# Performance work log

Measured on AMD Instinct MI355X. Metric: run time of the kernel, lower is better.

Reference implementation:

```python
import jax, jax.numpy as jnp
import numpy as np

WS = 8          # window_size
POOL = 7        # int(sqrt(agent_num=49)) -> AdaptiveAvgPool1d output size


def _pool_matrix(L, p):
    """Averaging matrix [L, p] replicating torch AdaptiveAvgPool1d(L -> p)."""
    starts = np.floor(np.arange(p) * L / p).astype(int)
    ends = np.ceil((np.arange(p) + 1) * L / p).astype(int)
    P = np.zeros((L, p), dtype=np.float32)
    for i in range(p):
        P[starts[i]:ends[i], i] = 1.0 / (ends[i] - starts[i])
    return jnp.asarray(P)


def setup_inputs() -> dict:
    key = jax.random.key(0)
    ks = jax.random.split(key, 4)
    B, C, H, W = 8, 96, 192, 192
    s = 1.0 / np.sqrt(C)
    return {
        "x": jax.random.normal(ks[0], (B, C, H, W), jnp.float32),
        "Wv": jax.random.normal(ks[1], (C, C), jnp.float32) * s,
        "bv": jnp.zeros((C,), jnp.float32),
        "Wq": jax.random.normal(ks[2], (C, C), jnp.float32) * s,
        "bq": jnp.zeros((C,), jnp.float32),
        "Wk": jax.random.normal(ks[3], (C, C), jnp.float32) * s,
        "bk": jnp.zeros((C,), jnp.float32),
    }


def _conv1x1(x, Wt, b):
    # Conv2d(dim, dim, 1): weight [out, in]
    return jnp.einsum('bchw,oc->bohw', x, Wt) + b[None, :, None, None]


def reference(x, Wv, bv, Wq, bq, Wk, bk):
    B, C, H, W = x.shape
    ws = WS
    nh, nw = H // ws, W // ws
    L = ws * ws  # tokens per window (64)

    v = _conv1x1(x, Wv, bv)
    q = _conv1x1(x, Wq, bq)
    k = _conv1x1(x, Wk, bk)

    def win(t):  # b c (h dh) (w dw) -> (b h w) (dh dw) c
        t = t.reshape(B, C, nh, ws, nw, ws)
        return t.transpose(0, 2, 4, 3, 5, 1).reshape(B * nh * nw, L, C)

    vw, qw, kw = win(v), win(q), win(k)  # (N, 64, C) each

    # agent tokens: adaptive avg pool over the 64 in-window positions -> 7
    P = _pool_matrix(L, POOL)
    agent = jnp.einsum('nlc,lp->npc', qw, P)  # (N, 7, C)

    # agent attention (attn_drop = 0 -> identity)
    a_attn = jax.nn.softmax(jnp.einsum('npc,nlc->npl', agent, kw), axis=-1)
    agent_v = jnp.einsum('npl,nlc->npc', a_attn, vw)            # (N, 7, C)
    q_attn = jax.nn.softmax(jnp.einsum('nlc,npc->nlp', qw, agent), axis=-1)
    f = jnp.einsum('nlp,npc->nlc', q_attn, agent_v)             # (N, 64, C)

    # (b h w) (dh dw) c -> b c (h dh) (w dw)
    out = f.reshape(B, nh, nw, ws, ws, C).transpose(0, 5, 1, 3, 2, 4)
    return out.reshape(B, C, H, W)
```

## Files before the change

### kernel.cpp

```cpp
#include <hip/hip_runtime.h>


constexpr int C_   = 96;
constexpr int Wimg = 192;
constexpr int HWp  = 192 * 192;
constexpr int NWIN = 24;
constexpr int Pp   = 7;

typedef __attribute__((ext_vector_type(8))) __bf16 bf16x8;
typedef __attribute__((ext_vector_type(4))) __bf16 bf16x4;
typedef __attribute__((ext_vector_type(8))) short  short8;
typedef __attribute__((ext_vector_type(4))) float  f32x4;
union frag_u { short8 s; bf16x8 b; };

constexpr int XWS   = 0;
constexpr int XWLC  = 12288;
constexpr int R1    = 24768;
constexpr int R2    = 31168;
constexpr int QATB  = 37568;
constexpr int SMEMB = 39872;

constexpr int WS_FRAG_BYTE = 18944 * 4;
constexpr int WS_WV_BYTE   = WS_FRAG_BYTE + 84 * 1024;


__device__ __forceinline__ void hilo8(const float4 a, const float4 b,
                                      frag_u& H, frag_u& L) {
    float v[8] = {a.x, a.y, a.z, a.w, b.x, b.y, b.z, b.w};
    #pragma unroll
    for (int j = 0; j < 8; ++j) {
        const __bf16 h = (__bf16)v[j];
        H.b[j] = h;
        L.b[j] = (__bf16)(v[j] - (float)h);
    }
}

__device__ __forceinline__ short8 xws_fragA(const unsigned char* S, int mt, int ks, int lane) {
    const int c  = mt * 16 + (lane & 15);
    const int l2 = ks * 64 + ((lane >> 4) << 4);
    return *reinterpret_cast<const short8*>(S + XWS + c * 128 + (l2 ^ ((c & 7) << 4)));
}


__global__ void precompute_mats(const float* __restrict__ Wq,
                                const float* __restrict__ Wk,
                                float* __restrict__ Mk,
                                float* __restrict__ Mq)
{
    const int c  = blockIdx.x;
    const int cp = threadIdx.x;
    float ak = 0.f, aq = 0.f;
    for (int a = 0; a < C_; ++a) {
        const float wq = Wq[a * C_ + c];
        ak = fmaf(wq, Wk[a * C_ + cp], ak);
        aq = fmaf(wq, Wq[a * C_ + cp], aq);
    }
    Mk[c * C_ + cp] = ak;
    Mq[c * C_ + cp] = aq;
}

__global__ void precompute_vecs(const float* __restrict__ Wq,
                                const float* __restrict__ Wk,
                                const float* __restrict__ bq,
                                const float* __restrict__ bk,
                                float* __restrict__ uk,  float* __restrict__ uq,
                                float* __restrict__ bk2, float* __restrict__ bq2,
                                float* __restrict__ scal)
{
    const int c = threadIdx.x;
    float a_uk = 0.f, a_uq = 0.f, a_bk2 = 0.f, a_bq2 = 0.f;
    for (int a = 0; a < C_; ++a) {
        const float wqc = Wq[a * C_ + c];
        a_uk  = fmaf(wqc, bk[a], a_uk);
        a_uq  = fmaf(wqc, bq[a], a_uq);
        a_bk2 = fmaf(bq[a], Wk[a * C_ + c], a_bk2);
        a_bq2 = fmaf(bq[a], Wq[a * C_ + c], a_bq2);
    }
    uk[c] = a_uk; uq[c] = a_uq; bk2[c] = a_bk2; bq2[c] = a_bq2;
    if (c == 0) {
        float sk = 0.f, sq = 0.f;
        for (int a = 0; a < C_; ++a) { sk += bq[a] * bk[a]; sq += bq[a] * bq[a]; }
        scal[0] = sk; scal[1] = sq;
    }
}

__global__ void precompute_frags(const float* __restrict__ ws,
                                 const float* __restrict__ Wv,
                                 unsigned char* __restrict__ wsb)
{
    const int bid = blockIdx.x, lane = threadIdx.x;
    short8 o;
    if (bid < 84) {
        const int hl = bid & 1, ks = (bid >> 1) % 3, nt = (bid / 6) % 7, mat = bid / 42;
        const float* M = ws + (mat ? 9216 : 0);
        const float* u = ws + (mat ? 18528 : 18432);
        const int col = nt * 16 + (lane & 15);
        #pragma unroll
        for (int j = 0; j < 8; ++j) {
            const int k = ks * 32 + (lane >> 4) * 8 + j;
            const float raw = (col < 96) ? M[k * 96 + col] : ((col == 96) ? u[k] : 0.f);
            const __bf16 hi = (__bf16)raw;
            union { __bf16 h; short s; } cv;
            cv.h = hl ? (__bf16)(raw - (float)hi) : hi;
            o[j] = cv.s;
        }
        *reinterpret_cast<short8*>(wsb + WS_FRAG_BYTE + bid * 1024 + lane * 16) = o;
    } else {
        const int wb = bid - 84;
        const int hl = wb & 1, ks = (wb >> 1) % 3, mt = wb / 6;
        const int row = mt * 16 + (lane & 15);
        #pragma unroll
        for (int j = 0; j < 8; ++j) {
            const int c = ks * 32 + (lane >> 4) * 8 + j;
            const float raw = Wv[row * 96 + c];
            const __bf16 hi = (__bf16)raw;
            union { __bf16 h; short s; } cv;
            cv.h = hl ? (__bf16)(raw - (float)hi) : hi;
            o[j] = cv.s;
        }
        *reinterpret_cast<short8*>(wsb + WS_WV_BYTE + wb * 1024 + lane * 16) = o;
    }
}


__global__ __launch_bounds__(256, 4) void camixer_main(
    const float* __restrict__ x,
    const float* __restrict__ bv,
    const float* __restrict__ bk2,
    const float* __restrict__ bq2,
    const float* __restrict__ scal,
    const unsigned char* __restrict__ mfrag,
    const unsigned char* __restrict__ wvfrag,
    float* __restrict__ out)
{
    __shared__ __align__(16) unsigned char S[SMEMB];
    float* xpf  = (float*)(S + R1);
    float* Lraw = (float*)(S + R1);
    float* xvf  = (float*)(S + R1);
    float* gkq  = (float*)(S + R2);
    float* avT  = (float*)(S + R2);
    float* qat  = (float*)(S + QATB);

    const int t = threadIdx.x;
    const int lane = t & 63, w = t >> 6;
    const int wid = ((blockIdx.x & 7) * 576) + (blockIdx.x >> 3);
    const int b  = wid / (NWIN * NWIN);
    const int r  = wid % (NWIN * NWIN);
    const int h0 = (r / NWIN) * 8;
    const int w0 = (r % NWIN) * 8;
    const int base = b * C_ * HWp + h0 * Wimg + w0;
    const float scal0 = scal[0], scal1 = scal[1];

    {
        const float4* x4 = reinterpret_cast<const float4*>(x);
        #pragma unroll
        for (int rr = 0; rr < 2; ++rr) {
            const int idx = t + (rr << 8);
            if (idx < 384) {
                const int dw4 = idx & 1;
                const int dh  = (idx >> 1) & 7;
                const int c4  = idx >> 4;
                const int c0 = c4 * 4, l0 = dh * 8 + dw4 * 4;
                __bf16 bf[4][4];
                #pragma unroll
                for (int j = 0; j < 4; ++j) {
                    const float4 v = x4[(base + (c0 + j) * HWp + dh * Wimg + dw4 * 4) >> 2];
                    bf[j][0] = (__bf16)v.x; bf[j][1] = (__bf16)v.y;
                    bf[j][2] = (__bf16)v.z; bf[j][3] = (__bf16)v.w;
                }
                #pragma unroll
                for (int j = 0; j < 4; ++j) {
                    const int c = c0 + j;
                    bf16x4 d = {bf[j][0], bf[j][1], bf[j][2], bf[j][3]};
                    *reinterpret_cast<bf16x4*>(S + XWS + c * 128 + ((l0 * 2) ^ ((c & 7) << 4))) = d;
                }
                #pragma unroll
                for (int i = 0; i < 4; ++i) {
                    const int l = l0 + i;
                    const int s = (c0 >> 5) * 4 + (l >> 4);
                    const int quad = (l & 15) + ((c0 >> 3) & 3) * 16;
                    bf16x4 d = {bf[0][i], bf[1][i], bf[2][i], bf[3][i]};
                    *reinterpret_cast<bf16x4*>(S + XWLC + s * 1040 + quad * 16 + (c0 & 7) * 2) = d;
                }
            }
        }
    }
    __syncthreads();

    {
        frag_u PAh[2], PAl[2];
        {
            const int p = lane & 15, kb = lane >> 4;
            const __bf16 PH = (__bf16)0.1f;
            const __bf16 PL = (__bf16)(0.1f - (float)PH);
            const int sp = (p < 7) ? ((p << 6) / 7) : 1000;
            #pragma unroll
            for (int ks = 0; ks < 2; ++ks)
                #pragma unroll
                for (int j = 0; j < 8; ++j) {
                    const int l = ks * 32 + kb * 8 + j;
                    const bool in = (l >= sp) && (l < sp + 10);
                    PAh[ks].b[j] = in ? PH : (__bf16)0.f;
                    PAl[ks].b[j] = in ? PL : (__bf16)0.f;
                }
        }
        #pragma unroll
        for (int rnd = 0; rnd < 2; ++rnd) {
            const int nt = rnd ? (4 + w) : w;
            if (rnd == 0 || w < 2) {
                f32x4 acc = {0.f, 0.f, 0.f, 0.f};
                #pragma unroll
                for (int ks = 0; ks < 2; ++ks) {
                    frag_u B;
                    B.s = xws_fragA(S, nt, ks, lane);
                    acc = __builtin_amdgcn_mfma_f32_16x16x32_bf16(PAh[ks].b, B.b, acc, 0, 0, 0);
                    acc = __builtin_amdgcn_mfma_f32_16x16x32_bf16(PAl[ks].b, B.b, acc, 0, 0, 0);
                }
                const int cc = nt * 16 + (lane & 15);
                #pragma unroll
                for (int rr = 0; rr < 4; ++rr)
                    xpf[((lane >> 4) * 4 + rr) * 100 + cc] = acc[rr];
            }
        }
    }
    __syncthreads();

    {
        frag_u Ah[3], Al[3];
        #pragma unroll
        for (int ks = 0; ks < 3; ++ks) {
            const int off = (lane & 15) * 100 + ks * 32 + (lane >> 4) * 8;
            hilo8(*reinterpret_cast<const float4*>(&xpf[off]),
                  *reinterpret_cast<const float4*>(&xpf[off + 4]), Ah[ks], Al[ks]);
        }
        #pragma unroll
        for (int rr4 = 0; rr4 < 4; ++rr4) {
            const int tt = w + 4 * rr4;
            if (tt < 14) {
                const int mat = tt / 7, nt = tt % 7;
                f32x4 acc = {0.f, 0.f, 0.f, 0.f};
                #pragma unroll
                for (int ks = 0; ks < 3; ++ks) {
                    const int slot = ((mat * 7 + nt) * 3 + ks) * 2;
                    frag_u Bh, Bl;
                    Bh.s = *reinterpret_cast<const short8*>(mfrag + slot * 1024 + (lane << 4));
                    Bl.s = *reinterpret_cast<const short8*>(mfrag + (slot + 1) * 1024 + (lane << 4));
                    acc = __builtin_amdgcn_mfma_f32_16x16x32_bf16(Ah[ks].b, Bh.b, acc, 0, 0, 0);
                    acc = __builtin_amdgcn_mfma_f32_16x16x32_bf16(Ah[ks].b, Bl.b, acc, 0, 0, 0);
                    acc = __builtin_amdgcn_mfma_f32_16x16x32_bf16(Al[ks].b, Bh.b, acc, 0, 0, 0);
                }
                const int row0 = (lane >> 4) * 4;
                if (nt < 6) {
                    const int cc = nt * 16 + (lane & 15);
                    const float b2v = (mat ? bq2 : bk2)[cc];
                    #pragma unroll
                    for (int rr = 0; rr < 4; ++rr) {
                        const int rw = row0 + rr;
                        if (rw < 8) gkq[(rw + 8 * mat) * 100 + cc] = acc[rr] + b2v;
                    }
                } else if ((lane & 15) == 0) {
                    #pragma unroll
                    for (int rr = 0; rr < 4; ++rr) {
                        const int rw = row0 + rr;
                        if (rw < 8) gkq[(rw + 8 * mat) * 100 + 96] = acc[rr];
                    }
                }
            }
        }
    }
    __syncthreads();

    {
        frag_u Ah[3], Al[3], B[3];
        #pragma unroll
        for (int ks = 0; ks < 3; ++ks) {
            const int off = (lane & 15) * 100 + ks * 32 + (lane >> 4) * 8;
            hilo8(*reinterpret_cast<const float4*>(&gkq[off]),
                  *reinterpret_cast<const float4*>(&gkq[off + 4]), Ah[ks], Al[ks]);
            B[ks].s = *reinterpret_cast<const short8*>(S + XWLC + (ks * 4 + w) * 1040 + (lane << 4));
        }
        f32x4 acc = {0.f, 0.f, 0.f, 0.f};
        #pragma unroll
        for (int ks = 0; ks < 3; ++ks) {
            acc = __builtin_amdgcn_mfma_f32_16x16x32_bf16(Ah[ks].b, B[ks].b, acc, 0, 0, 0);
            acc = __builtin_amdgcn_mfma_f32_16x16x32_bf16(Al[ks].b, B[ks].b, acc, 0, 0, 0);
        }
        const int colL = w * 16 + (lane & 15);
        #pragma unroll
        for (int rr = 0; rr < 4; ++rr) {
            const int pr = (lane >> 4) * 4 + rr;
            const float bias = gkq[pr * 100 + 96] + (pr < 8 ? scal0 : scal1);
            Lraw[pr * 66 + colL] = acc[rr] + bias;
        }
    }
    __syncthreads();

    if (w < 3) {
        #pragma unroll
        for (int rr = 0; rr < 2; ++rr) {
            const int pp = w + 3 * rr;
            const float v = Lraw[pp * 66 + lane];
            float mx = v;
            #pragma unroll
            for (int off = 32; off; off >>= 1) mx = fmaxf(mx, __shfl_xor(mx, off));
            const float e = __expf(v - mx);
            float s = e;
            #pragma unroll
            for (int off = 32; off; off >>= 1) s += __shfl_xor(s, off);
            const float a = e / s;
            const __bf16 hb = (__bf16)a;
            const __bf16 lb = (__bf16)(a - (float)hb);
            const int ks = lane >> 5;
            const int off_b = ((pp + 16 * ((lane >> 3) & 3)) << 4) + ((lane & 7) << 1);
            *reinterpret_cast<__bf16*>(S + R2 + (ks << 10) + off_b) = hb;
            *reinterpret_cast<__bf16*>(S + R2 + ((2 + ks) << 10) + off_b) = lb;
        }
    } else {
        {
            const int pp = 6;
            const float v = Lraw[pp * 66 + lane];
            float mx = v;
            #pragma unroll
            for (int off = 32; off; off >>= 1) mx = fmaxf(mx, __shfl_xor(mx, off));
            const float e = __expf(v - mx);
            float s = e;
            #pragma unroll
            for (int off = 32; off; off >>= 1) s += __shfl_xor(s, off);
            const float a = e / s;
            const __bf16 hb = (__bf16)a;
            const __bf16 lb = (__bf16)(a - (float)hb);
            const int ks = lane >> 5;
            const int off_b = ((pp + 16 * ((lane >> 3) & 3)) << 4) + ((lane & 7) << 1);
            *reinterpret_cast<__bf16*>(S + R2 + (ks << 10) + off_b) = hb;
            *reinterpret_cast<__bf16*>(S + R2 + ((2 + ks) << 10) + off_b) = lb;
        }
        float vv[Pp];
        float mx = -1e30f;
        #pragma unroll
        for (int p = 0; p < Pp; ++p) { vv[p] = Lraw[(8 + p) * 66 + lane]; mx = fmaxf(mx, vv[p]); }
        float s = 0.f;
        #pragma unroll
        for (int p = 0; p < Pp; ++p) { vv[p] = __expf(vv[p] - mx); s += vv[p]; }
        const float inv = 1.f / s;
        #pragma unroll
        for (int p = 0; p < Pp; ++p) qat[lane * 9 + p] = vv[p] * inv;
    }
    __syncthreads();

    {
        frag_u Bh[2], Bl[2];
        #pragma unroll
        for (int ks = 0; ks < 2; ++ks) {
            Bh[ks].s = *reinterpret_cast<const short8*>(S + R2 + (ks << 10) + (lane << 4));
            Bl[ks].s = *reinterpret_cast<const short8*>(S + R2 + ((2 + ks) << 10) + (lane << 4));
        }
        const int mt0 = (w < 2) ? w * 2 : (w + 2);
        const int nmt = (w < 2) ? 2 : 1;
        for (int m = 0; m < nmt; ++m) {
            const int mt = mt0 + m;
            f32x4 acc = {0.f, 0.f, 0.f, 0.f};
            #pragma unroll
            for (int ks = 0; ks < 2; ++ks) {
                frag_u A;
                A.s = xws_fragA(S, mt, ks, lane);
                acc = __builtin_amdgcn_mfma_f32_16x16x32_bf16(A.b, Bh[ks].b, acc, 0, 0, 0);
                acc = __builtin_amdgcn_mfma_f32_16x16x32_bf16(A.b, Bl[ks].b, acc, 0, 0, 0);
            }
            const int p = lane & 15;
            const int c0 = mt * 16 + (lane >> 4) * 4;
            *reinterpret_cast<f32x4*>(&xvf[p * 100 + c0]) = acc;
        }
    }
    __syncthreads();

    {
        frag_u Bh[3], Bl[3];
        #pragma unroll
        for (int ks = 0; ks < 3; ++ks) {
            const int off = (lane & 15) * 100 + ks * 32 + (lane >> 4) * 8;
            hilo8(*reinterpret_cast<const float4*>(&xvf[off]),
                  *reinterpret_cast<const float4*>(&xvf[off + 4]), Bh[ks], Bl[ks]);
        }
        #pragma unroll
        for (int rnd = 0; rnd < 2; ++rnd) {
            const int mt = rnd ? (4 + w) : w;
            if (rnd == 0 || w < 2) {
                f32x4 acc = {0.f, 0.f, 0.f, 0.f};
                #pragma unroll
                for (int ks = 0; ks < 3; ++ks) {
                    const int slot = (mt * 3 + ks) * 2;
                    frag_u Ah, Al;
                    Ah.s = *reinterpret_cast<const short8*>(wvfrag + slot * 1024 + (lane << 4));
                    Al.s = *reinterpret_cast<const short8*>(wvfrag + (slot + 1) * 1024 + (lane << 4));
                    acc = __builtin_amdgcn_mfma_f32_16x16x32_bf16(Ah.b, Bh[ks].b, acc, 0, 0, 0);
                    acc = __builtin_amdgcn_mfma_f32_16x16x32_bf16(Ah.b, Bl[ks].b, acc, 0, 0, 0);
                    acc = __builtin_amdgcn_mfma_f32_16x16x32_bf16(Al.b, Bh[ks].b, acc, 0, 0, 0);
                }
                if ((lane & 15) < 8) {
                    #pragma unroll
                    for (int rr = 0; rr < 4; ++rr) {
                        const int o = mt * 16 + (lane >> 4) * 4 + rr;
                        avT[o * 8 + (lane & 15)] = acc[rr] + bv[o];
                    }
                }
            }
        }
    }
    __syncthreads();

    {
        float qa[Pp];
        #pragma unroll
        for (int p = 0; p < Pp; ++p) qa[p] = qat[lane * 9 + p];
        const int dh = lane >> 3, dw = lane & 7;
        const int obase = b * C_ * HWp + (h0 + dh) * Wimg + (w0 + dw);
        #pragma unroll 4
        for (int j = 0; j < 24; ++j) {
            const int o = w + 4 * j;
            const float4 a0 = *reinterpret_cast<const float4*>(&avT[o * 8]);
            const float4 a1 = *reinterpret_cast<const float4*>(&avT[o * 8 + 4]);
            float acc = qa[0] * a0.x;
            acc = fmaf(qa[1], a0.y, acc);
            acc = fmaf(qa[2], a0.z, acc);
            acc = fmaf(qa[3], a0.w, acc);
            acc = fmaf(qa[4], a1.x, acc);
            acc = fmaf(qa[5], a1.y, acc);
            acc = fmaf(qa[6], a1.z, acc);
            out[obase + o * HWp] = acc;
        }
    }
}


extern "C" void kernel_launch(void* const* d_in, const int* in_sizes, int n_in,
                              void* d_out, int out_size, void* d_ws, size_t ws_size,
                              hipStream_t stream)
{
    const float* x  = (const float*)d_in[0];
    const float* Wv = (const float*)d_in[1];
    const float* bv = (const float*)d_in[2];
    const float* Wq = (const float*)d_in[3];
    const float* bq = (const float*)d_in[4];
    const float* Wk = (const float*)d_in[5];
    const float* bk = (const float*)d_in[6];
    float* out = (float*)d_out;

    float* ws = (float*)d_ws;
    float* Mk   = ws;
    float* Mq   = ws + 9216;
    float* uk   = ws + 18432;
    float* uq   = ws + 18528;
    float* bk2  = ws + 18624;
    float* bq2  = ws + 18720;
    float* scal = ws + 18816;
    unsigned char* wsb = (unsigned char*)d_ws;

    hipLaunchKernelGGL(precompute_mats, dim3(C_), dim3(C_), 0, stream,
                       Wq, Wk, Mk, Mq);
    hipLaunchKernelGGL(precompute_vecs, dim3(1), dim3(C_), 0, stream,
                       Wq, Wk, bq, bk, uk, uq, bk2, bq2, scal);
    hipLaunchKernelGGL(precompute_frags, dim3(120), dim3(64), 0, stream,
                       ws, Wv, wsb);
    hipLaunchKernelGGL(camixer_main, dim3(8 * NWIN * NWIN), dim3(256), 0, stream,
                       x, bv, bk2, bq2, scal,
                       wsb + WS_FRAG_BYTE, wsb + WS_WV_BYTE, out);
}
```

Measured before the change: 89.06 us.

## Prefetch weight fragments early and use lighter LDS-only barriers

Global loads of the precomputed K/Q and V weight fragments are issued before the phases that use them: the first K/Q tile is loaded at kernel entry, later tiles are software-pipelined with the MFMA work, and the V fragments are loaded before the preceding stage. __syncthreads is replaced by an lgkmcnt(0) wait plus s_barrier, so barriers no longer drain outstanding global loads. The aim is to hide global and L2 latency on the fragment tables. The cost is higher register pressure under launch_bounds(256,4), and every barrier now depends on no cross-wave global-memory visibility being needed.

```diff
diff --git a/kernel.cpp b/kernel.cpp
--- a/kernel.cpp
+++ b/kernel.cpp
@@ -23,6 +23,11 @@
 constexpr int WS_FRAG_BYTE = 18944 * 4;
 constexpr int WS_WV_BYTE   = WS_FRAG_BYTE + 84 * 1024;
 
+
+__device__ __forceinline__ void bar() {
+    asm volatile("s_waitcnt lgkmcnt(0)" ::: "memory");
+    __builtin_amdgcn_s_barrier();
+}
 
 __device__ __forceinline__ void hilo8(const float4 a, const float4 b,
                                       frag_u& H, frag_u& L) {
@@ -121,6 +126,11 @@
         *reinterpret_cast<short8*>(wsb + WS_WV_BYTE + wb * 1024 + lane * 16) = o;
     }
 }
+
+#define LOADPAIR(dstH, dstL, tab, slot_h) do {                                        \
+    (dstH).s = *reinterpret_cast<const short8*>((tab) + (slot_h) * 1024 + (lane << 4));      \
+    (dstL).s = *reinterpret_cast<const short8*>((tab) + ((slot_h) + 1) * 1024 + (lane << 4));\
+} while (0)
 
 
 __global__ __launch_bounds__(256, 4) void camixer_main(
@@ -150,6 +160,11 @@
     const int w0 = (r % NWIN) * 8;
     const int base = b * C_ * HWp + h0 * Wimg + w0;
     const float scal0 = scal[0], scal1 = scal[1];
+
+    frag_u B0h[3], B0l[3];
+    LOADPAIR(B0h[0], B0l[0], mfrag, (w * 3 + 0) * 2);
+    LOADPAIR(B0h[1], B0l[1], mfrag, (w * 3 + 1) * 2);
+    LOADPAIR(B0h[2], B0l[2], mfrag, (w * 3 + 2) * 2);
 
     {
         const float4* x4 = reinterpret_cast<const float4*>(x);
@@ -185,7 +200,7 @@
             }
         }
     }
-    __syncthreads();
+    bar();
 
     {
         frag_u PAh[2], PAl[2];
@@ -223,7 +238,7 @@
             }
         }
     }
-    __syncthreads();
+    bar();
 
     {
         frag_u Ah[3], Al[3];
@@ -233,51 +248,70 @@
             hilo8(*reinterpret_cast<const float4*>(&xpf[off]),
                   *reinterpret_cast<const float4*>(&xpf[off + 4]), Ah[ks], Al[ks]);
         }
-        #pragma unroll
-        for (int rr4 = 0; rr4 < 4; ++rr4) {
-            const int tt = w + 4 * rr4;
-            if (tt < 14) {
-                const int mat = tt / 7, nt = tt % 7;
-                f32x4 acc = {0.f, 0.f, 0.f, 0.f};
-                #pragma unroll
-                for (int ks = 0; ks < 3; ++ks) {
-                    const int slot = ((mat * 7 + nt) * 3 + ks) * 2;
-                    frag_u Bh, Bl;
-                    Bh.s = *reinterpret_cast<const short8*>(mfrag + slot * 1024 + (lane << 4));
-                    Bl.s = *reinterpret_cast<const short8*>(mfrag + (slot + 1) * 1024 + (lane << 4));
-                    acc = __builtin_amdgcn_mfma_f32_16x16x32_bf16(Ah[ks].b, Bh.b, acc, 0, 0, 0);
-                    acc = __builtin_amdgcn_mfma_f32_16x16x32_bf16(Ah[ks].b, Bl.b, acc, 0, 0, 0);
-                    acc = __builtin_amdgcn_mfma_f32_16x16x32_bf16(Al[ks].b, Bh.b, acc, 0, 0, 0);
-                }
-                const int row0 = (lane >> 4) * 4;
-                if (nt < 6) {
-                    const int cc = nt * 16 + (lane & 15);
-                    const float b2v = (mat ? bq2 : bk2)[cc];
-                    #pragma unroll
-                    for (int rr = 0; rr < 4; ++rr) {
-                        const int rw = row0 + rr;
-                        if (rw < 8) gkq[(rw + 8 * mat) * 100 + cc] = acc[rr] + b2v;
-                    }
-                } else if ((lane & 15) == 0) {
-                    #pragma unroll
-                    for (int rr = 0; rr < 4; ++rr) {
-                        const int rw = row0 + rr;
-                        if (rw < 8) gkq[(rw + 8 * mat) * 100 + 96] = acc[rr];
-                    }
-                }
-            }
-        }
-    }
-    __syncthreads();
-
-    {
-        frag_u Ah[3], Al[3], B[3];
+
+        #define G0TILE(TT, BH, BL) do {                                               \
+            const int tt_ = (TT);                                                     \
+            const int mat_ = (tt_ >= 7) ? 1 : 0;                                      \
+            const int nt_  = tt_ - 7 * mat_;                                          \
+            f32x4 acc = {0.f, 0.f, 0.f, 0.f};                                         \
+            acc = __builtin_amdgcn_mfma_f32_16x16x32_bf16(Ah[0].b, BH[0].b, acc, 0,0,0); \
+            acc = __builtin_amdgcn_mfma_f32_16x16x32_bf16(Ah[0].b, BL[0].b, acc, 0,0,0); \
+            acc = __builtin_amdgcn_mfma_f32_16x16x32_bf16(Al[0].b, BH[0].b, acc, 0,0,0); \
+            acc = __builtin_amdgcn_mfma_f32_16x16x32_bf16(Ah[1].b, BH[1].b, acc, 0,0,0); \
+            acc = __builtin_amdgcn_mfma_f32_16x16x32_bf16(Ah[1].b, BL[1].b, acc, 0,0,0); \
+            acc = __builtin_amdgcn_mfma_f32_16x16x32_bf16(Al[1].b, BH[1].b, acc, 0,0,0); \
+            acc = __builtin_amdgcn_mfma_f32_16x16x32_bf16(Ah[2].b, BH[2].b, acc, 0,0,0); \
+            acc = __builtin_amdgcn_mfma_f32_16x16x32_bf16(Ah[2].b, BL[2].b, acc, 0,0,0); \
+            acc = __builtin_amdgcn_mfma_f32_16x16x32_bf16(Al[2].b, BH[2].b, acc, 0,0,0); \
+            const int row0_ = (lane >> 4) * 4;                                        \
+            if (nt_ < 6) {                                                            \
+                const int cc_ = nt_ * 16 + (lane & 15);                               \
+                const float b2v_ = (mat_ ? bq2 : bk2)[cc_];                           \
+                _Pragma("unroll")                                                     \
+                for (int rr = 0; rr < 4; ++rr) {                                      \
+                    const int rw_ = row0_ + rr;                                       \
+                    if (rw_ < 8) gkq[(rw_ + 8 * mat_) * 100 + cc_] = acc[rr] + b2v_;  \
+                }                                                                     \
+            } else if ((lane & 15) == 0) {                                            \
+                _Pragma("unroll")                                                     \
+                for (int rr = 0; rr < 4; ++rr) {                                      \
+                    const int rw_ = row0_ + rr;                                       \
+                    if (rw_ < 8) gkq[(rw_ + 8 * mat_) * 100 + 96] = acc[rr];          \
+                }                                                                     \
+            }                                                                         \
+        } while (0)
+
+        frag_u B1h[3], B1l[3], B2h[3], B2l[3], B3h[3], B3l[3];
+        LOADPAIR(B1h[0], B1l[0], mfrag, (((w + 4) % 7 + 7 * ((w + 4) / 7)) * 3 + 0) * 2);
+        LOADPAIR(B1h[1], B1l[1], mfrag, ((w + 4) * 3 + 1) * 2);
+        LOADPAIR(B1h[2], B1l[2], mfrag, ((w + 4) * 3 + 2) * 2);
+        G0TILE(w, B0h, B0l);
+        LOADPAIR(B2h[0], B2l[0], mfrag, ((w + 8) * 3 + 0) * 2);
+        LOADPAIR(B2h[1], B2l[1], mfrag, ((w + 8) * 3 + 1) * 2);
+        LOADPAIR(B2h[2], B2l[2], mfrag, ((w + 8) * 3 + 2) * 2);
+        G0TILE(w + 4, B1h, B1l);
+        if (w < 2) {
+            LOADPAIR(B3h[0], B3l[0], mfrag, ((w + 12) * 3 + 0) * 2);
+            LOADPAIR(B3h[1], B3l[1], mfrag, ((w + 12) * 3 + 1) * 2);
+            LOADPAIR(B3h[2], B3l[2], mfrag, ((w + 12) * 3 + 2) * 2);
+        }
+        G0TILE(w + 8, B2h, B2l);
+        if (w < 2) G0TILE(w + 12, B3h, B3l);
+        #undef G0TILE
+    }
+    bar();
+
+    {
+        frag_u B[3];
+        #pragma unroll
+        for (int ks = 0; ks < 3; ++ks)
+            B[ks].s = *reinterpret_cast<const short8*>(S + XWLC + (ks * 4 + w) * 1040 + (lane << 4));
+        frag_u Ah[3], Al[3];
         #pragma unroll
         for (int ks = 0; ks < 3; ++ks) {
             const int off = (lane & 15) * 100 + ks * 32 + (lane >> 4) * 8;
             hilo8(*reinterpret_cast<const float4*>(&gkq[off]),
                   *reinterpret_cast<const float4*>(&gkq[off + 4]), Ah[ks], Al[ks]);
-            B[ks].s = *reinterpret_cast<const short8*>(S + XWLC + (ks * 4 + w) * 1040 + (lane << 4));
         }
         f32x4 acc = {0.f, 0.f, 0.f, 0.f};
         #pragma unroll
@@ -293,7 +327,7 @@
             Lraw[pr * 66 + colL] = acc[rr] + bias;
         }
     }
-    __syncthreads();
+    bar();
 
     if (w < 3) {
         #pragma unroll
@@ -345,9 +379,19 @@
         #pragma unroll
         for (int p = 0; p < Pp; ++p) qat[lane * 9 + p] = vv[p] * inv;
     }
-    __syncthreads();
-
-    {
+    bar();
+
+    frag_u V0h[3], V0l[3], V1h[3], V1l[3];
+    {
+        LOADPAIR(V0h[0], V0l[0], wvfrag, (w * 3 + 0) * 2);
+        LOADPAIR(V0h[1], V0l[1], wvfrag, (w * 3 + 1) * 2);
+        LOADPAIR(V0h[2], V0l[2], wvfrag, (w * 3 + 2) * 2);
+        if (w < 2) {
+            LOADPAIR(V1h[0], V1l[0], wvfrag, ((4 + w) * 3 + 0) * 2);
+            LOADPAIR(V1h[1], V1l[1], wvfrag, ((4 + w) * 3 + 1) * 2);
+            LOADPAIR(V1h[2], V1l[2], wvfrag, ((4 + w) * 3 + 2) * 2);
+        }
+
         frag_u Bh[2], Bl[2];
         #pragma unroll
         for (int ks = 0; ks < 2; ++ks) {
@@ -371,7 +415,7 @@
             *reinterpret_cast<f32x4*>(&xvf[p * 100 + c0]) = acc;
         }
     }
-    __syncthreads();
+    bar();
 
     {
         frag_u Bh[3], Bl[3];
@@ -381,32 +425,30 @@
             hilo8(*reinterpret_cast<const float4*>(&xvf[off]),
                   *reinterpret_cast<const float4*>(&xvf[off + 4]), Bh[ks], Bl[ks]);
         }
-        #pragma unroll
-        for (int rnd = 0; rnd < 2; ++rnd) {
-            const int mt = rnd ? (4 + w) : w;
-            if (rnd == 0 || w < 2) {
-                f32x4 acc = {0.f, 0.f, 0.f, 0.f};
-                #pragma unroll
-                for (int ks = 0; ks < 3; ++ks) {
-                    const int slot = (mt * 3 + ks) * 2;
-                    frag_u Ah, Al;
-                    Ah.s = *reinterpret_cast<const short8*>(wvfrag + slot * 1024 + (lane << 4));
-                    Al.s = *reinterpret_cast<const short8*>(wvfrag + (slot + 1) * 1024 + (lane << 4));
-                    acc = __builtin_amdgcn_mfma_f32_16x16x32_bf16(Ah.b, Bh[ks].b, acc, 0, 0, 0);
-                    acc = __builtin_amdgcn_mfma_f32_16x16x32_bf16(Ah.b, Bl[ks].b, acc, 0, 0, 0);
-                    acc = __builtin_amdgcn_mfma_f32_16x16x32_bf16(Al.b, Bh[ks].b, acc, 0, 0, 0);
-                }
-                if ((lane & 15) < 8) {
-                    #pragma unroll
-                    for (int rr = 0; rr < 4; ++rr) {
-                        const int o = mt * 16 + (lane >> 4) * 4 + rr;
-                        avT[o * 8 + (lane & 15)] = acc[rr] + bv[o];
-                    }
-                }
-            }
-        }
-    }
-    __syncthreads();
+        #define G3TILE(MT, VH, VL) do {                                               \
+            f32x4 acc = {0.f, 0.f, 0.f, 0.f};                                         \
+            acc = __builtin_amdgcn_mfma_f32_16x16x32_bf16(VH[0].b, Bh[0].b, acc, 0,0,0); \
+            acc = __builtin_amdgcn_mfma_f32_16x16x32_bf16(VH[0].b, Bl[0].b, acc, 0,0,0); \
+            acc = __builtin_amdgcn_mfma_f32_16x16x32_bf16(VL[0].b, Bh[0].b, acc, 0,0,0); \
+            acc = __builtin_amdgcn_mfma_f32_16x16x32_bf16(VH[1].b, Bh[1].b, acc, 0,0,0); \
+            acc = __builtin_amdgcn_mfma_f32_16x16x32_bf16(VH[1].b, Bl[1].b, acc, 0,0,0); \
+            acc = __builtin_amdgcn_mfma_f32_16x16x32_bf16(VL[1].b, Bh[1].b, acc, 0,0,0); \
+            acc = __builtin_amdgcn_mfma_f32_16x16x32_bf16(VH[2].b, Bh[2].b, acc, 0,0,0); \
+            acc = __builtin_amdgcn_mfma_f32_16x16x32_bf16(VH[2].b, Bl[2].b, acc, 0,0,0); \
+            acc = __builtin_amdgcn_mfma_f32_16x16x32_bf16(VL[2].b, Bh[2].b, acc, 0,0,0); \
+            if ((lane & 15) < 8) {                                                    \
+                _Pragma("unroll")                                                     \
+                for (int rr = 0; rr < 4; ++rr) {                                      \
+                    const int o_ = (MT) * 16 + (lane >> 4) * 4 + rr;                  \
+                    avT[o_ * 8 + (lane & 15)] = acc[rr] + bv[o_];                     \
+                }                                                                     \
+            }                                                                         \
+        } while (0)
+        G3TILE(w, V0h, V0l);
+        if (w < 2) G3TILE(4 + w, V1h, V1l);
+        #undef G3TILE
+    }
+    bar();
 
     {
         float qa[Pp];
```

New measurement: 81.99 us. 1.09x faster.
